# Kernel tuning notes

Measured on AMD Instinct MI355X. Metric: run time of the kernel, lower is better.

Reference implementation:

```python
import jax, jax.numpy as jnp
import numpy as np

NUM_HEADS = 8
DIM_HEAD = 64
HEIGHT_TOP_K = 256
WIDTH_TOP_K = 256


def setup_inputs() -> dict:
    key = jax.random.key(0)
    k1, k2, k3 = jax.random.split(key, 3)
    B, N, C = 4, 2048, 512
    x = jax.random.normal(k1, (B, N, C), dtype=jnp.float32)
    w_qkv = jax.random.normal(k2, (C, 3 * C), dtype=jnp.float32) * (C ** -0.5)
    w_out = jax.random.normal(k3, (C, C), dtype=jnp.float32) * (C ** -0.5)
    b_out = jnp.zeros((C,), dtype=jnp.float32)
    return {"x": x, "w_qkv": w_qkv, "w_out": w_out, "b_out": b_out}


def _topk_mask(scores, k):
    # scores: (B, H, N) -> binary mask (B, H, N) with 1s at top-k positions
    N = scores.shape[-1]
    _, idx = jax.lax.top_k(scores, k)          # (B, H, k)
    # indices are distinct, so summing one-hots == scatter set(1)
    return jax.nn.one_hot(idx, N, dtype=scores.dtype).sum(axis=-2)


def reference(x, w_qkv, w_out, b_out):
    B, N, C = x.shape
    H, D = NUM_HEADS, DIM_HEAD
    scale = D ** -0.5

    qkv = x @ w_qkv                             # (B, N, 3C)
    q, k, v = jnp.split(qkv, 3, axis=-1)
    # (B, N, C) -> (B, H, N, D)
    q = q.reshape(B, N, H, D).transpose(0, 2, 1, 3)
    k = k.reshape(B, N, H, D).transpose(0, 2, 1, 3)
    v = v.reshape(B, N, H, D).transpose(0, 2, 1, 3)

    attn = jnp.einsum('bhid,bhjd->bhij', q, k) * scale   # (B, H, N, N)

    hk = min(HEIGHT_TOP_K, N)
    wk = min(WIDTH_TOP_K, N)
    row_mask = _topk_mask(attn.mean(axis=-1), hk)        # (B, H, N)
    col_mask = _topk_mask(attn.mean(axis=-2), wk)        # (B, H, N)
    attn = attn * row_mask[..., :, None] * col_mask[..., None, :]

    attn = jax.nn.softmax(attn, axis=-1)
    out = jnp.einsum('bhij,bhjd->bhid', attn, v)         # (B, H, N, D)
    out = out.transpose(0, 2, 1, 3).reshape(B, N, C)
    return out @ w_out + b_out
```

## Files before the change

kernel.cpp:

```cpp
#include <hip/hip_runtime.h>
#include <math.h>

#define Bsz 4
#define Nseq 2048
#define Cdim 512
#define Hn 8
#define Dh 64
#define TK 256
#define BH (Bsz*Hn)
#define QKVC 1536

typedef __attribute__((ext_vector_type(8))) short bf16x8;
typedef __attribute__((ext_vector_type(4))) float f32x4;

__device__ __forceinline__ unsigned short f2bf(float x) {
    unsigned u = __float_as_uint(x);
    unsigned r = (u + 0x7fffu + ((u >> 16) & 1u)) >> 16;
    return (unsigned short)r;
}
__device__ __forceinline__ float bf2f(unsigned short h) {
    return __uint_as_float((unsigned)h << 16);
}

__global__ __launch_bounds__(256) void prep(const float* __restrict__ w_qkv,
                                            bf16x8* __restrict__ hi,
                                            bf16x8* __restrict__ lo,
                                            const float* __restrict__ x,
                                            float* __restrict__ xpart) {
    int bid = blockIdx.x;
    int tid = threadIdx.x;
    if (bid < 384) {
        int nt = bid >> 2;
        int kt = (bid & 3) * 4 + (tid >> 6);
        int lane = tid & 63;
        int c = nt * 16 + (lane & 15);
        int kbase = kt * 32 + (lane >> 4) * 8;
        bf16x8 h, l;
        #pragma unroll
        for (int j = 0; j < 8; ++j) {
            float v = w_qkv[(size_t)(kbase + j) * QKVC + c];
            unsigned short hv = f2bf(v);
            h[j] = (short)hv;
            l[j] = (short)f2bf(v - bf2f(hv));
        }
        int idx = (nt * 16 + kt) * 64 + lane;
        hi[idx] = h;
        lo[idx] = l;
    } else {
        int r = bid - 384;
        int b = r >> 7, rc = r & 127;
        const float* xp = x + ((size_t)b * Nseq + rc * 16) * Cdim;
        float s0 = 0.f, s1 = 0.f;
        #pragma unroll 4
        for (int rr = 0; rr < 16; ++rr) {
            s0 += xp[rr * Cdim + tid];
            s1 += xp[rr * Cdim + 256 + tid];
        }
        xpart[((size_t)b * 128 + rc) * Cdim + tid] = s0;
        xpart[((size_t)b * 128 + rc) * Cdim + 256 + tid] = s1;
    }
}

__global__ __launch_bounds__(256) void statsA(const float* __restrict__ xpart,
                                              const float* __restrict__ w_qkv,
                                              float* __restrict__ spart) {
    int b = blockIdx.x, kc = blockIdx.y, nb = blockIdx.z;
    __shared__ float xr[8][32];
    __shared__ float xs[32];
    int t = threadIdx.x;
    int i = t & 31, g = t >> 5;
    float s = 0.f;
    #pragma unroll 4
    for (int j = 0; j < 16; ++j)
        s += xpart[((size_t)b * 128 + g * 16 + j) * Cdim + kc * 32 + i];
    xr[g][i] = s;
    __syncthreads();
    if (t < 32) {
        float v = 0.f;
        #pragma unroll
        for (int gg = 0; gg < 8; ++gg) v += xr[gg][t];
        xs[t] = v;
    }
    __syncthreads();

    float a0 = 0.f;
    const float* wbase = w_qkv + (size_t)(kc * 32) * QKVC + nb * 256 + t;
    #pragma unroll 4
    for (int i2 = 0; i2 < 32; ++i2)
        a0 += xs[i2] * wbase[(size_t)i2 * QKVC];
    spart[(size_t)(b * 16 + kc) * QKVC + nb * 256 + t] = a0;
}

__global__ __launch_bounds__(256) void statsB(const float* __restrict__ spart,
                                              const float* __restrict__ w_qkv,
                                              float* __restrict__ sv,
                                              float* __restrict__ rvec,
                                              float* __restrict__ cvec) {
    int bh = blockIdx.x, cb = blockIdx.y;
    int b = bh >> 3, h = bh & 7;
    __shared__ float qm[64], km[64];
    int t = threadIdx.x;
    if (t < 192) {
        int which = t >> 6, d = t & 63;
        int col = which * 512 + h * 64 + d;
        float s = 0.f;
        #pragma unroll
        for (int kc = 0; kc < 16; ++kc)
            s += spart[(size_t)(b * 16 + kc) * QKVC + col];
        if (which == 0)      qm[d] = s * (1.0f / Nseq);
        else if (which == 1) km[d] = s * (1.0f / Nseq);
        else if (cb == 0)    sv[bh * 64 + d] = s;
    }
    __syncthreads();
    int c = cb * 256 + t;
    const float4* wr = (const float4*)(w_qkv + (size_t)c * QKVC + h * 64);
    const float4* wc = (const float4*)(w_qkv + (size_t)c * QKVC + 512 + h * 64);
    float r = 0.f, cv = 0.f;
    #pragma unroll
    for (int d4 = 0; d4 < 16; ++d4) {
        float4 w1 = wr[d4], w2 = wc[d4];
        float4 k1 = *(const float4*)&km[d4 * 4];
        float4 q1 = *(const float4*)&qm[d4 * 4];
        r  += w1.x * k1.x + w1.y * k1.y + w1.z * k1.z + w1.w * k1.w;
        cv += w2.x * q1.x + w2.y * q1.y + w2.z * q1.z + w2.w * q1.w;
    }
    rvec[(size_t)bh * Cdim + c] = r;
    cvec[(size_t)bh * Cdim + c] = cv;
}

__global__ __launch_bounds__(256) void score3_kernel(const float* __restrict__ x,
                                                     const float* __restrict__ rvec,
                                                     const float* __restrict__ cvec,
                                                     float* __restrict__ rsc,
                                                     float* __restrict__ csc) {
    int b = blockIdx.x, rc = blockIdx.y, half = blockIdx.z;
    __shared__ float vs[8 * 8 * 68];
    int t = threadIdx.x;
    int r = t >> 3, g = t & 7;

    const float4* xp = (const float4*)(x + ((size_t)b * Nseq + rc * 32 + r) * Cdim + g * 64);
    float4 xr[16];
    #pragma unroll
    for (int j4 = 0; j4 < 16; ++j4) xr[j4] = xp[j4];

    {
        const float* src = half ? cvec : rvec;
        const float4* sp = (const float4*)(src + (size_t)b * 8 * Cdim);
        for (int i = t; i < 8 * 128; i += 256) {
            int v = i >> 7, c4 = i & 127;
            float4 val = sp[v * 128 + c4];
            int gg = c4 >> 4, j4 = c4 & 15;
            *(float4*)&vs[(v * 8 + gg) * 68 + j4 * 4] = val;
        }
    }
    __syncthreads();

    float acc[8];
    #pragma unroll
    for (int v = 0; v < 8; ++v) acc[v] = 0.f;
    #pragma unroll
    for (int j4 = 0; j4 < 16; ++j4) {
        float4 xv = xr[j4];
        #pragma unroll
        for (int v = 0; v < 8; ++v) {
            float4 wv = *(const float4*)&vs[(v * 8 + g) * 68 + j4 * 4];
            acc[v] += xv.x * wv.x + xv.y * wv.y + xv.z * wv.z + xv.w * wv.w;
        }
    }
    #pragma unroll
    for (int v = 0; v < 8; ++v) {
        float s = acc[v];
        s += __shfl_xor(s, 1, 64);
        s += __shfl_xor(s, 2, 64);
        s += __shfl_xor(s, 4, 64);
        acc[v] = s;
    }
    if (g == 0) {
        int i = rc * 32 + r;
        float* outp = half ? csc : rsc;
        #pragma unroll
        for (int v = 0; v < 8; ++v)
            outp[(size_t)(b * 8 + v) * Nseq + i] = acc[v] * 0.125f;
    }
}

__global__ __launch_bounds__(256) void topk4(const float* __restrict__ rsc,
                                             const float* __restrict__ csc,
                                             int* __restrict__ ridx,
                                             int* __restrict__ cidx,
                                             int* __restrict__ rankmap) {
    int selid = blockIdx.x;
    int bh = selid >> 1, which = selid & 1;
    const float* sin = which ? (csc + (size_t)bh * Nseq) : (rsc + (size_t)bh * Nseq);
    __shared__ int hist[256];
    __shared__ int sS[256];
    __shared__ int tieidx[2048];
    __shared__ int sh_D, sh_above, sh_tiecnt;
    int tid = threadIdx.x;

    unsigned k[8];
    #pragma unroll
    for (int j = 0; j < 8; ++j) {
        unsigned u = __float_as_uint(sin[j * 256 + tid]);
        k[j] = (u & 0x80000000u) ? ~u : (u | 0x80000000u);
    }

    unsigned pref = 0;
    int above = 0;
    for (int level = 3; level >= 0; --level) {
        hist[tid] = 0;
        __syncthreads();
        int sh = level * 8;
        #pragma unroll
        for (int j = 0; j < 8; ++j) {
            bool match;
            if (level == 3) match = true;
            else            match = ((k[j] >> (sh + 8)) == pref);
            if (match) atomicAdd(&hist[(k[j] >> sh) & 255], 1);
        }
        __syncthreads();
        sS[tid] = hist[tid];
        __syncthreads();
        for (int off = 1; off < 256; off <<= 1) {
            int v = (tid + off < 256) ? sS[tid + off] : 0;
            __syncthreads();
            sS[tid] += v;
            __syncthreads();
        }
        int Sincl = sS[tid];
        int Sexcl = (tid < 255) ? sS[tid + 1] : 0;
        if (above + Sexcl < TK && above + Sincl >= TK) {
            sh_D = tid;
            sh_above = above + Sexcl;
        }
        __syncthreads();
        pref = (pref << 8) | (unsigned)sh_D;
        above = sh_above;
        __syncthreads();
    }
    unsigned T = pref;
    int rem = TK - above;

    if (tid == 0) sh_tiecnt = 0;
    __syncthreads();
    int cnt = 0;
    #pragma unroll
    for (int j = 0; j < 8; ++j) {
        if (k[j] > T) ++cnt;
        if (k[j] == T) {
            int p = atomicAdd(&sh_tiecnt, 1);
            tieidx[p] = j * 256 + tid;
        }
    }
    sS[tid] = cnt;
    __syncthreads();
    for (int off = 1; off < 256; off <<= 1) {
        int v = (tid >= off) ? sS[tid - off] : 0;
        __syncthreads();
        sS[tid] += v;
        __syncthreads();
    }
    int base = sS[tid] - cnt;
    int tc = sh_tiecnt;
    int* outp = which ? (cidx + bh * TK) : (ridx + bh * TK);
    #pragma unroll
    for (int j = 0; j < 8; ++j) {
        int i = j * 256 + tid;
        int r = -1;
        if (k[j] > T) {
            r = base++;
        } else if (k[j] == T) {
            int rk = 0;
            for (int t2 = 0; t2 < tc; ++t2) rk += (tieidx[t2] < i) ? 1 : 0;
            if (rk < rem) r = above + rk;
        }
        if (r >= 0) outp[r] = i;
        if (which == 0) rankmap[(size_t)bh * Nseq + i] = r;
    }
}

__device__ __forceinline__ f32x4 mfma16(bf16x8 a, bf16x8 b, f32x4 c) {
    return __builtin_amdgcn_mfma_f32_16x16x32_bf16(a, b, c, 0, 0, 0);
}

__global__ __launch_bounds__(256) void selgemm3(const float* __restrict__ x,
                                                const int* __restrict__ ridx,
                                                const int* __restrict__ cidx,
                                                const bf16x8* __restrict__ Bph,
                                                const bf16x8* __restrict__ Bpl,
                                                float* __restrict__ qsel,
                                                float* __restrict__ ksel,
                                                float* __restrict__ vsel) {
    int mq = blockIdx.x, part = blockIdx.y, bh = blockIdx.z;
    int b = bh >> 3, h = bh & 7;
    int tid = threadIdx.x;
    int wv = tid >> 6, lane = tid & 63;
    const int* idxp = (part == 0 ? ridx : cidx) + bh * TK + mq * 64 + wv * 16;
    int row = idxp[lane & 15];
    const float* ap = x + ((size_t)b * Nseq + row) * Cdim + (lane >> 4) * 8;
    size_t orow = (size_t)bh * TK + mq * 64 + wv * 16;
    int nt0 = (part == 0) ? (h * 4) : (part == 1 ? (32 + h * 4) : (64 + h * 4));
    float* outp = (part == 0) ? qsel : (part == 1 ? ksel : vsel);

    f32x4 acc[4];
    #pragma unroll
    for (int i = 0; i < 4; ++i) acc[i] = (f32x4){0.f, 0.f, 0.f, 0.f};
    float4 a0 = *(const float4*)ap;
    float4 a1 = *(const float4*)(ap + 4);
    #pragma unroll 2
    for (int kt = 0; kt < 16; ++kt) {
        float4 na0 = a0, na1 = a1;
        if (kt < 15) {
            na0 = *(const float4*)(ap + (kt + 1) * 32);
            na1 = *(const float4*)(ap + (kt + 1) * 32 + 4);
        }
        float vv[8] = {a0.x, a0.y, a0.z, a0.w, a1.x, a1.y, a1.z, a1.w};
        bf16x8 ah, al;
        #pragma unroll
        for (int j = 0; j < 8; ++j) {
            unsigned short hv = f2bf(vv[j]);
            ah[j] = (short)hv;
            al[j] = (short)f2bf(vv[j] - bf2f(hv));
        }
        #pragma unroll
        for (int ni = 0; ni < 4; ++ni) {
            int nt16 = nt0 + ni;
            bf16x8 bh8 = Bph[((size_t)nt16 * 16 + kt) * 64 + lane];
            bf16x8 bl8 = Bpl[((size_t)nt16 * 16 + kt) * 64 + lane];
            acc[ni] = mfma16(ah, bh8, acc[ni]);
            acc[ni] = mfma16(ah, bl8, acc[ni]);
            acc[ni] = mfma16(al, bh8, acc[ni]);
        }
        a0 = na0; a1 = na1;
    }
    int cl = lane & 15, rq = (lane >> 4) * 4;
    #pragma unroll
    for (int ni = 0; ni < 4; ++ni) {
        int csub = ni * 16 + cl;
        #pragma unroll
        for (int r = 0; r < 4; ++r)
            outp[(orow + rq + r) * 64 + csub] = acc[ni][r];
    }
}

__global__ __launch_bounds__(256) void attn_fused3(const float* __restrict__ qsel,
                                                   const float* __restrict__ ksel,
                                                   const float* __restrict__ vsel,
                                                   const float* __restrict__ sv,
                                                   float* __restrict__ delta) {
    int bh = blockIdx.x;
    int rblk = blockIdx.y;
    __shared__ float Kt[64 * 256];
    __shared__ float Qs[16 * 64];
    __shared__ float umS[16], izS[16];
    int tid = threadIdx.x;
    {
        int j = tid;
        const float4* kp4 = (const float4*)(ksel + ((size_t)bh * TK + j) * 64);
        #pragma unroll
        for (int d4 = 0; d4 < 16; ++d4) {
            float4 kv = kp4[d4];
            Kt[(d4 * 4 + 0) * 256 + j] = kv.x;
            Kt[(d4 * 4 + 1) * 256 + j] = kv.y;
            Kt[(d4 * 4 + 2) * 256 + j] = kv.z;
            Kt[(d4 * 4 + 3) * 256 + j] = kv.w;
        }
    }
    for (int idx = tid; idx < 16 * 64; idx += 256)
        Qs[idx] = qsel[((size_t)bh * TK + rblk * 16) * 64 + idx];
    __syncthreads();

    int wave = tid >> 6, lane = tid & 63;
    int iw0 = wave * 4;
    float e[4][4];
    #pragma unroll
    for (int r = 0; r < 4; ++r)
        #pragma unroll
        for (int t = 0; t < 4; ++t) e[r][t] = 0.f;
    #pragma unroll 8
    for (int d = 0; d < 64; ++d) {
        float4 kv = *(const float4*)&Kt[d * 256 + 4 * lane];
        #pragma unroll
        for (int r = 0; r < 4; ++r) {
            float qd = Qs[(iw0 + r) * 64 + d];
            e[r][0] += qd * kv.x; e[r][1] += qd * kv.y;
            e[r][2] += qd * kv.z; e[r][3] += qd * kv.w;
        }
    }
    #pragma unroll
    for (int r = 0; r < 4; ++r) {
        float s0 = e[r][0] * 0.125f, s1 = e[r][1] * 0.125f;
        float s2 = e[r][2] * 0.125f, s3 = e[r][3] * 0.125f;
        float mx = fmaxf(fmaxf(s0, s1), fmaxf(s2, s3));
        #pragma unroll
        for (int off = 32; off; off >>= 1) mx = fmaxf(mx, __shfl_xor(mx, off, 64));
        mx = fmaxf(mx, 0.0f);
        float e0 = __expf(s0 - mx), e1 = __expf(s1 - mx);
        float e2 = __expf(s2 - mx), e3 = __expf(s3 - mx);
        float zs = e0 + e1 + e2 + e3;
        #pragma unroll
        for (int off = 32; off; off >>= 1) zs += __shfl_xor(zs, off, 64);
        if (lane == 0) {
            float em = __expf(-mx);
            umS[iw0 + r] = em;
            izS[iw0 + r] = 1.0f / ((float)(Nseq - TK) * em + zs);
        }
        e[r][0] = e0; e[r][1] = e1; e[r][2] = e2; e[r][3] = e3;
    }
    __syncthreads();
    float* E = Kt;
    #pragma unroll
    for (int r = 0; r < 4; ++r)
        *(float4*)&E[(iw0 + r) * 256 + 4 * lane] = (float4){e[r][0], e[r][1], e[r][2], e[r][3]};
    __syncthreads();

    const float* vbase = vsel + (size_t)bh * TK * 64 + lane;
    float ssel = 0.f;
    float acc[4];
    #pragma unroll
    for (int r = 0; r < 4; ++r) acc[r] = 0.f;
    #pragma unroll 4
    for (int j = 0; j < TK; ++j) {
        float v = vbase[j * 64];
        ssel += v;
        #pragma unroll
        for (int r = 0; r < 4; ++r)
            acc[r] += E[(iw0 + r) * 256 + j] * v;
    }
    float svd = sv[bh * 64 + lane];
    float sadj = svd - ssel;
    float uval = svd * (1.0f / Nseq);
    #pragma unroll
    for (int r = 0; r < 4; ++r) {
        int i = rblk * 16 + iw0 + r;
        float outv = (umS[iw0 + r] * sadj + acc[r]) * izS[iw0 + r];
        delta[((size_t)bh * TK + i) * 64 + lane] = outv - uval;
    }
}

__global__ __launch_bounds__(256) void deltamm_ub(const float* __restrict__ delta,
                                                  const float* __restrict__ w_out,
                                                  const float* __restrict__ b_out,
                                                  const float* __restrict__ sv,
                                                  float* __restrict__ deltaout,
                                                  float* __restrict__ ubase) {
    int bid = blockIdx.x;
    int tid = threadIdx.x;
    if (bid < 512) {
        int bh = bid >> 4, sub = bid & 15;
        int rh = sub >> 2, ct = sub & 3;
        int h = bh & 7;
        __shared__ float As[64][65];
        __shared__ float Ws[64][132];
        for (int idx = tid; idx < 64 * 64; idx += 256) {
            int row = idx >> 6, k = idx & 63;
            As[row][k] = delta[((size_t)bh * TK + rh * 64 + row) * 64 + k];
        }
        for (int idx = tid; idx < 64 * 128; idx += 256) {
            int k = idx >> 7, c = idx & 127;
            Ws[k][c] = w_out[(size_t)(h * 64 + k) * 512 + ct * 128 + c];
        }
        __syncthreads();
        int tx = tid & 15, ty = tid >> 4;
        float acc[4][8];
        #pragma unroll
        for (int r = 0; r < 4; ++r)
            #pragma unroll
            for (int c = 0; c < 8; ++c) acc[r][c] = 0.f;
        for (int k = 0; k < 64; ++k) {
            float a[4], bv[8];
            #pragma unroll
            for (int r = 0; r < 4; ++r) a[r] = As[ty * 4 + r][k];
            #pragma unroll
            for (int cc = 0; cc < 4; ++cc) {
                bv[cc]     = Ws[k][tx * 4 + cc];
                bv[4 + cc] = Ws[k][64 + tx * 4 + cc];
            }
            #pragma unroll
            for (int r = 0; r < 4; ++r)
                #pragma unroll
                for (int c = 0; c < 8; ++c) acc[r][c] += a[r] * bv[c];
        }
        #pragma unroll
        for (int r = 0; r < 4; ++r) {
            size_t ro = ((size_t)bh * TK + rh * 64 + ty * 4 + r) * 512 + ct * 128;
            #pragma unroll
            for (int cc = 0; cc < 4; ++cc) {
                deltaout[ro + tx * 4 + cc]      = acc[r][cc];
                deltaout[ro + 64 + tx * 4 + cc] = acc[r][4 + cc];
            }
        }
    } else {
        int r2 = bid - 512;
        int b = r2 >> 3;
        int c0 = (r2 & 7) * 64;
        int c = tid & 63, kg = tid >> 6;
        float s = 0.f;
        for (int k = kg * 128; k < kg * 128 + 128; ++k) {
            float hu = sv[(b * 8 + (k >> 6)) * 64 + (k & 63)] * (1.0f / Nseq);
            s += hu * w_out[(size_t)k * 512 + c0 + c];
        }
        __shared__ float red[4][64];
        red[kg][c] = s;
        __syncthreads();
        if (tid < 64)
            ubase[b * 512 + c0 + c] = red[0][c] + red[1][c] + red[2][c] + red[3][c] + b_out[c0 + c];
    }
}

__global__ __launch_bounds__(256) void compose(const float* __restrict__ ubase,
                                               const int* __restrict__ rankmap,
                                               const float* __restrict__ deltaout,
                                               float* __restrict__ out) {
    int r0 = blockIdx.x * 4;
    int b = r0 >> 11;
    int tid = threadIdx.x;
    float u0 = ubase[b * 512 + tid];
    float u1 = ubase[b * 512 + 256 + tid];
    for (int rr = 0; rr < 4; ++rr) {
        int i = (r0 + rr) & 2047;
        float a0 = u0, a1 = u1;
        #pragma unroll
        for (int h = 0; h < 8; ++h) {
            int rk = rankmap[(size_t)(b * 8 + h) * Nseq + i];
            if (rk >= 0) {
                const float* dp = deltaout + ((size_t)(b * 8 + h) * TK + rk) * 512;
                a0 += dp[tid];
                a1 += dp[256 + tid];
            }
        }
        float* op = out + ((size_t)b * Nseq + i) * 512;
        op[tid] = a0;
        op[256 + tid] = a1;
    }
}

extern "C" void kernel_launch(void* const* d_in, const int* in_sizes, int n_in,
                              void* d_out, int out_size, void* d_ws, size_t ws_size,
                              hipStream_t stream) {
    const float* x     = (const float*)d_in[0];
    const float* w_qkv = (const float*)d_in[1];
    const float* w_out = (const float*)d_in[2];
    const float* b_out = (const float*)d_in[3];
    float* out = (float*)d_out;

    float* ws = (float*)d_ws;
    float* xpart   = ws;
    float* spart   = xpart + 262144;
    float* sv      = spart + 98304;
    float* rvec    = sv + 2048;
    float* cvec    = rvec + 16384;
    float* rsc     = cvec + 16384;
    float* csc     = rsc + 65536;
    int*   ridx    = (int*)(csc + 65536);
    int*   cidx    = ridx + 8192;
    int*   rankmap = cidx + 8192;
    float* ubase   = (float*)(rankmap + 65536);
    bf16x8* Bp_hi  = (bf16x8*)(ubase + 2048);
    bf16x8* Bp_lo  = (bf16x8*)((float*)Bp_hi + 393216);
    float* qsel    = (float*)Bp_lo + 393216;
    float* ksel    = qsel + 524288;
    float* vsel    = ksel + 524288;
    float* delta   = vsel + 524288;
    float* deltaout = delta + 524288;

    prep<<<896, 256, 0, stream>>>(w_qkv, Bp_hi, Bp_lo, x, xpart);
    statsA<<<dim3(Bsz, 16, 6), 256, 0, stream>>>(xpart, w_qkv, spart);
    statsB<<<dim3(BH, 2), 256, 0, stream>>>(spart, w_qkv, sv, rvec, cvec);
    score3_kernel<<<dim3(Bsz, 64, 2), 256, 0, stream>>>(x, rvec, cvec, rsc, csc);
    topk4<<<BH * 2, 256, 0, stream>>>(rsc, csc, ridx, cidx, rankmap);
    selgemm3<<<dim3(4, 3, BH), 256, 0, stream>>>(x, ridx, cidx, Bp_hi, Bp_lo, qsel, ksel, vsel);
    attn_fused3<<<dim3(BH, 16), 256, 0, stream>>>(qsel, ksel, vsel, sv, delta);
    deltamm_ub<<<544, 256, 0, stream>>>(delta, w_out, b_out, sv, deltaout, ubase);
    compose<<<Bsz * Nseq / 4, 256, 0, stream>>>(ubase, rankmap, deltaout, out);
}
```

Baseline: 172.5 us.

## Fuse all pipeline stages into one cooperative persistent kernel with grid syncs

Turns each of the nine stage kernels into a device function and runs them in sequence inside one cooperative kernel. Stages are separated by grid.sync, and blocks stride over each stage's work units. Shared memory is a union of the per-stage layouts. This removes eight kernel launch gaps and their tail drains, at the cost of grid-wide barriers, occupancy being capped by the largest shared-memory footprint (the attention stage's 68KB), and fewer blocks than some stages have work units. If the cooperative launch fails, the separate kernels are launched as before.

```diff
diff --git a/kernel.cpp b/kernel.cpp
--- a/kernel.cpp
+++ b/kernel.cpp
@@ -1,5 +1,8 @@
 #include <hip/hip_runtime.h>
+#include <hip/hip_cooperative_groups.h>
 #include <math.h>
+
+namespace cg = cooperative_groups;
 
 #define Bsz 4
 #define Nseq 2048
@@ -21,17 +24,28 @@
 __device__ __forceinline__ float bf2f(unsigned short h) {
     return __uint_as_float((unsigned)h << 16);
 }
-
-__global__ __launch_bounds__(256) void prep(const float* __restrict__ w_qkv,
-                                            bf16x8* __restrict__ hi,
-                                            bf16x8* __restrict__ lo,
-                                            const float* __restrict__ x,
-                                            float* __restrict__ xpart) {
-    int bid = blockIdx.x;
+__device__ __forceinline__ f32x4 mfma16(bf16x8 a, bf16x8 b, f32x4 c) {
+    return __builtin_amdgcn_mfma_f32_16x16x32_bf16(a, b, c, 0, 0, 0);
+}
+
+struct S2Sh { float xr[8][32]; float xs[32]; };
+struct S3Sh { float qm[64]; float km[64]; };
+struct S4Sh { float vs[8 * 8 * 68]; };
+struct S5Sh { int hist[256]; int sS[256]; int tieidx[2048]; int D; int above; int tiecnt; };
+struct S7Sh { float Kt[64 * 256]; float Qs[16 * 64]; float umS[16]; float izS[16]; };
+struct S8Sh { float As[64][65]; float Ws[64][132]; float red[4][64]; };
+union FusedSh {
+    S2Sh s2; S3Sh s3; S4Sh s4; S5Sh s5; S7Sh s7; S8Sh s8;
+};
+
+
+__device__ void prep_body(int u, const float* __restrict__ w_qkv,
+                          bf16x8* __restrict__ hi, bf16x8* __restrict__ lo,
+                          const float* __restrict__ x, float* __restrict__ xpart) {
     int tid = threadIdx.x;
-    if (bid < 384) {
-        int nt = bid >> 2;
-        int kt = (bid & 3) * 4 + (tid >> 6);
+    if (u < 384) {
+        int nt = u >> 2;
+        int kt = (u & 3) * 4 + (tid >> 6);
         int lane = tid & 63;
         int c = nt * 16 + (lane & 15);
         int kbase = kt * 32 + (lane >> 4) * 8;
@@ -47,7 +61,7 @@
         hi[idx] = h;
         lo[idx] = l;
     } else {
-        int r = bid - 384;
+        int r = u - 384;
         int b = r >> 7, rc = r & 127;
         const float* xp = x + ((size_t)b * Nseq + rc * 16) * Cdim;
         float s0 = 0.f, s1 = 0.f;
@@ -61,55 +75,50 @@
     }
 }
 
-__global__ __launch_bounds__(256) void statsA(const float* __restrict__ xpart,
-                                              const float* __restrict__ w_qkv,
-                                              float* __restrict__ spart) {
-    int b = blockIdx.x, kc = blockIdx.y, nb = blockIdx.z;
-    __shared__ float xr[8][32];
-    __shared__ float xs[32];
+__device__ void statsA_body(int u, const float* __restrict__ xpart,
+                            const float* __restrict__ w_qkv,
+                            float* __restrict__ spart, S2Sh& s) {
+    int b = u & 3, kc = (u >> 2) & 15, nb = u >> 6;
     int t = threadIdx.x;
     int i = t & 31, g = t >> 5;
-    float s = 0.f;
+    float acc = 0.f;
     #pragma unroll 4
     for (int j = 0; j < 16; ++j)
-        s += xpart[((size_t)b * 128 + g * 16 + j) * Cdim + kc * 32 + i];
-    xr[g][i] = s;
+        acc += xpart[((size_t)b * 128 + g * 16 + j) * Cdim + kc * 32 + i];
+    s.xr[g][i] = acc;
     __syncthreads();
     if (t < 32) {
         float v = 0.f;
         #pragma unroll
-        for (int gg = 0; gg < 8; ++gg) v += xr[gg][t];
-        xs[t] = v;
-    }
-    __syncthreads();
-
+        for (int gg = 0; gg < 8; ++gg) v += s.xr[gg][t];
+        s.xs[t] = v;
+    }
+    __syncthreads();
     float a0 = 0.f;
     const float* wbase = w_qkv + (size_t)(kc * 32) * QKVC + nb * 256 + t;
     #pragma unroll 4
     for (int i2 = 0; i2 < 32; ++i2)
-        a0 += xs[i2] * wbase[(size_t)i2 * QKVC];
+        a0 += s.xs[i2] * wbase[(size_t)i2 * QKVC];
     spart[(size_t)(b * 16 + kc) * QKVC + nb * 256 + t] = a0;
 }
 
-__global__ __launch_bounds__(256) void statsB(const float* __restrict__ spart,
-                                              const float* __restrict__ w_qkv,
-                                              float* __restrict__ sv,
-                                              float* __restrict__ rvec,
-                                              float* __restrict__ cvec) {
-    int bh = blockIdx.x, cb = blockIdx.y;
+__device__ void statsB_body(int u, const float* __restrict__ spart,
+                            const float* __restrict__ w_qkv,
+                            float* __restrict__ sv, float* __restrict__ rvec,
+                            float* __restrict__ cvec, S3Sh& s) {
+    int bh = u & 31, cb = u >> 5;
     int b = bh >> 3, h = bh & 7;
-    __shared__ float qm[64], km[64];
     int t = threadIdx.x;
     if (t < 192) {
         int which = t >> 6, d = t & 63;
         int col = which * 512 + h * 64 + d;
-        float s = 0.f;
+        float sm = 0.f;
         #pragma unroll
         for (int kc = 0; kc < 16; ++kc)
-            s += spart[(size_t)(b * 16 + kc) * QKVC + col];
-        if (which == 0)      qm[d] = s * (1.0f / Nseq);
-        else if (which == 1) km[d] = s * (1.0f / Nseq);
-        else if (cb == 0)    sv[bh * 64 + d] = s;
+            sm += spart[(size_t)(b * 16 + kc) * QKVC + col];
+        if (which == 0)      s.qm[d] = sm * (1.0f / Nseq);
+        else if (which == 1) s.km[d] = sm * (1.0f / Nseq);
+        else if (cb == 0)    sv[bh * 64 + d] = sm;
     }
     __syncthreads();
     int c = cb * 256 + t;
@@ -119,8 +128,8 @@
     #pragma unroll
     for (int d4 = 0; d4 < 16; ++d4) {
         float4 w1 = wr[d4], w2 = wc[d4];
-        float4 k1 = *(const float4*)&km[d4 * 4];
-        float4 q1 = *(const float4*)&qm[d4 * 4];
+        float4 k1 = *(const float4*)&s.km[d4 * 4];
+        float4 q1 = *(const float4*)&s.qm[d4 * 4];
         r  += w1.x * k1.x + w1.y * k1.y + w1.z * k1.z + w1.w * k1.w;
         cv += w2.x * q1.x + w2.y * q1.y + w2.z * q1.z + w2.w * q1.w;
     }
@@ -128,21 +137,18 @@
     cvec[(size_t)bh * Cdim + c] = cv;
 }
 
-__global__ __launch_bounds__(256) void score3_kernel(const float* __restrict__ x,
-                                                     const float* __restrict__ rvec,
-                                                     const float* __restrict__ cvec,
-                                                     float* __restrict__ rsc,
-                                                     float* __restrict__ csc) {
-    int b = blockIdx.x, rc = blockIdx.y, half = blockIdx.z;
-    __shared__ float vs[8 * 8 * 68];
+__device__ void score3_body(int u, const float* __restrict__ x,
+                            const float* __restrict__ rvec,
+                            const float* __restrict__ cvec,
+                            float* __restrict__ rsc, float* __restrict__ csc,
+                            S4Sh& s) {
+    int b = u & 3, rc = (u >> 2) & 63, half = u >> 8;
     int t = threadIdx.x;
     int r = t >> 3, g = t & 7;
-
     const float4* xp = (const float4*)(x + ((size_t)b * Nseq + rc * 32 + r) * Cdim + g * 64);
     float4 xr[16];
     #pragma unroll
     for (int j4 = 0; j4 < 16; ++j4) xr[j4] = xp[j4];
-
     {
         const float* src = half ? cvec : rvec;
         const float4* sp = (const float4*)(src + (size_t)b * 8 * Cdim);
@@ -150,11 +156,10 @@
             int v = i >> 7, c4 = i & 127;
             float4 val = sp[v * 128 + c4];
             int gg = c4 >> 4, j4 = c4 & 15;
-            *(float4*)&vs[(v * 8 + gg) * 68 + j4 * 4] = val;
-        }
-    }
-    __syncthreads();
-
+            *(float4*)&s.vs[(v * 8 + gg) * 68 + j4 * 4] = val;
+        }
+    }
+    __syncthreads();
     float acc[8];
     #pragma unroll
     for (int v = 0; v < 8; ++v) acc[v] = 0.f;
@@ -163,17 +168,17 @@
         float4 xv = xr[j4];
         #pragma unroll
         for (int v = 0; v < 8; ++v) {
-            float4 wv = *(const float4*)&vs[(v * 8 + g) * 68 + j4 * 4];
+            float4 wv = *(const float4*)&s.vs[(v * 8 + g) * 68 + j4 * 4];
             acc[v] += xv.x * wv.x + xv.y * wv.y + xv.z * wv.z + xv.w * wv.w;
         }
     }
     #pragma unroll
     for (int v = 0; v < 8; ++v) {
-        float s = acc[v];
-        s += __shfl_xor(s, 1, 64);
-        s += __shfl_xor(s, 2, 64);
-        s += __shfl_xor(s, 4, 64);
-        acc[v] = s;
+        float sm = acc[v];
+        sm += __shfl_xor(sm, 1, 64);
+        sm += __shfl_xor(sm, 2, 64);
+        sm += __shfl_xor(sm, 4, 64);
+        acc[v] = sm;
     }
     if (g == 0) {
         int i = rc * 32 + r;
@@ -184,31 +189,23 @@
     }
 }
 
-__global__ __launch_bounds__(256) void topk4(const float* __restrict__ rsc,
-                                             const float* __restrict__ csc,
-                                             int* __restrict__ ridx,
-                                             int* __restrict__ cidx,
-                                             int* __restrict__ rankmap) {
-    int selid = blockIdx.x;
-    int bh = selid >> 1, which = selid & 1;
+__device__ void topk4_body(int u, const float* __restrict__ rsc,
+                           const float* __restrict__ csc,
+                           int* __restrict__ ridx, int* __restrict__ cidx,
+                           int* __restrict__ rankmap, S5Sh& s) {
+    int bh = u >> 1, which = u & 1;
     const float* sin = which ? (csc + (size_t)bh * Nseq) : (rsc + (size_t)bh * Nseq);
-    __shared__ int hist[256];
-    __shared__ int sS[256];
-    __shared__ int tieidx[2048];
-    __shared__ int sh_D, sh_above, sh_tiecnt;
     int tid = threadIdx.x;
-
     unsigned k[8];
     #pragma unroll
     for (int j = 0; j < 8; ++j) {
-        unsigned u = __float_as_uint(sin[j * 256 + tid]);
-        k[j] = (u & 0x80000000u) ? ~u : (u | 0x80000000u);
-    }
-
+        unsigned uu = __float_as_uint(sin[j * 256 + tid]);
+        k[j] = (uu & 0x80000000u) ? ~uu : (uu | 0x80000000u);
+    }
     unsigned pref = 0;
     int above = 0;
     for (int level = 3; level >= 0; --level) {
-        hist[tid] = 0;
+        s.hist[tid] = 0;
         __syncthreads();
         int sh = level * 8;
         #pragma unroll
@@ -216,52 +213,51 @@
             bool match;
             if (level == 3) match = true;
             else            match = ((k[j] >> (sh + 8)) == pref);
-            if (match) atomicAdd(&hist[(k[j] >> sh) & 255], 1);
-        }
-        __syncthreads();
-        sS[tid] = hist[tid];
+            if (match) atomicAdd(&s.hist[(k[j] >> sh) & 255], 1);
+        }
+        __syncthreads();
+        s.sS[tid] = s.hist[tid];
         __syncthreads();
         for (int off = 1; off < 256; off <<= 1) {
-            int v = (tid + off < 256) ? sS[tid + off] : 0;
+            int v = (tid + off < 256) ? s.sS[tid + off] : 0;
             __syncthreads();
-            sS[tid] += v;
+            s.sS[tid] += v;
             __syncthreads();
         }
-        int Sincl = sS[tid];
-        int Sexcl = (tid < 255) ? sS[tid + 1] : 0;
+        int Sincl = s.sS[tid];
+        int Sexcl = (tid < 255) ? s.sS[tid + 1] : 0;
         if (above + Sexcl < TK && above + Sincl >= TK) {
-            sh_D = tid;
-            sh_above = above + Sexcl;
-        }
-        __syncthreads();
-        pref = (pref << 8) | (unsigned)sh_D;
-        above = sh_above;
+            s.D = tid;
+            s.above = above + Sexcl;
+        }
+        __syncthreads();
+        pref = (pref << 8) | (unsigned)s.D;
+        above = s.above;
         __syncthreads();
     }
     unsigned T = pref;
     int rem = TK - above;
-
-    if (tid == 0) sh_tiecnt = 0;
+    if (tid == 0) s.tiecnt = 0;
     __syncthreads();
     int cnt = 0;
     #pragma unroll
     for (int j = 0; j < 8; ++j) {
         if (k[j] > T) ++cnt;
         if (k[j] == T) {
-            int p = atomicAdd(&sh_tiecnt, 1);
-            tieidx[p] = j * 256 + tid;
-        }
-    }
-    sS[tid] = cnt;
+            int p = atomicAdd(&s.tiecnt, 1);
+            s.tieidx[p] = j * 256 + tid;
+        }
+    }
+    s.sS[tid] = cnt;
     __syncthreads();
     for (int off = 1; off < 256; off <<= 1) {
-        int v = (tid >= off) ? sS[tid - off] : 0;
-        __syncthreads();
-        sS[tid] += v;
-        __syncthreads();
-    }
-    int base = sS[tid] - cnt;
-    int tc = sh_tiecnt;
+        int v = (tid >= off) ? s.sS[tid - off] : 0;
+        __syncthreads();
+        s.sS[tid] += v;
+        __syncthreads();
+    }
+    int base = s.sS[tid] - cnt;
+    int tc = s.tiecnt;
     int* outp = which ? (cidx + bh * TK) : (ridx + bh * TK);
     #pragma unroll
     for (int j = 0; j < 8; ++j) {
@@ -271,7 +267,7 @@
             r = base++;
         } else if (k[j] == T) {
             int rk = 0;
-            for (int t2 = 0; t2 < tc; ++t2) rk += (tieidx[t2] < i) ? 1 : 0;
+            for (int t2 = 0; t2 < tc; ++t2) rk += (s.tieidx[t2] < i) ? 1 : 0;
             if (rk < rem) r = above + rk;
         }
         if (r >= 0) outp[r] = i;
@@ -279,19 +275,15 @@
     }
 }
 
-__device__ __forceinline__ f32x4 mfma16(bf16x8 a, bf16x8 b, f32x4 c) {
-    return __builtin_amdgcn_mfma_f32_16x16x32_bf16(a, b, c, 0, 0, 0);
-}
-
-__global__ __launch_bounds__(256) void selgemm3(const float* __restrict__ x,
-                                                const int* __restrict__ ridx,
-                                                const int* __restrict__ cidx,
-                                                const bf16x8* __restrict__ Bph,
-                                                const bf16x8* __restrict__ Bpl,
-                                                float* __restrict__ qsel,
-                                                float* __restrict__ ksel,
-                                                float* __restrict__ vsel) {
-    int mq = blockIdx.x, part = blockIdx.y, bh = blockIdx.z;
+__device__ void selgemm3_body(int u, const float* __restrict__ x,
+                              const int* __restrict__ ridx,
+                              const int* __restrict__ cidx,
+                              const bf16x8* __restrict__ Bph,
+                              const bf16x8* __restrict__ Bpl,
+                              float* __restrict__ qsel,
+                              float* __restrict__ ksel,
+                              float* __restrict__ vsel) {
+    int mq = u & 3, part = (u >> 2) % 3, bh = (u >> 2) / 3;
     int b = bh >> 3, h = bh & 7;
     int tid = threadIdx.x;
     int wv = tid >> 6, lane = tid & 63;
@@ -343,16 +335,12 @@
     }
 }
 
-__global__ __launch_bounds__(256) void attn_fused3(const float* __restrict__ qsel,
-                                                   const float* __restrict__ ksel,
-                                                   const float* __restrict__ vsel,
-                                                   const float* __restrict__ sv,
-                                                   float* __restrict__ delta) {
-    int bh = blockIdx.x;
-    int rblk = blockIdx.y;
-    __shared__ float Kt[64 * 256];
-    __shared__ float Qs[16 * 64];
-    __shared__ float umS[16], izS[16];
+__device__ void attn_body(int u, const float* __restrict__ qsel,
+                          const float* __restrict__ ksel,
+                          const float* __restrict__ vsel,
+                          const float* __restrict__ sv,
+                          float* __restrict__ delta, S7Sh& s) {
+    int bh = u & 31, rblk = u >> 5;
     int tid = threadIdx.x;
     {
         int j = tid;
@@ -360,14 +348,14 @@
         #pragma unroll
         for (int d4 = 0; d4 < 16; ++d4) {
             float4 kv = kp4[d4];
-            Kt[(d4 * 4 + 0) * 256 + j] = kv.x;
-            Kt[(d4 * 4 + 1) * 256 + j] = kv.y;
-            Kt[(d4 * 4 + 2) * 256 + j] = kv.z;
-            Kt[(d4 * 4 + 3) * 256 + j] = kv.w;
+            s.Kt[(d4 * 4 + 0) * 256 + j] = kv.x;
+            s.Kt[(d4 * 4 + 1) * 256 + j] = kv.y;
+            s.Kt[(d4 * 4 + 2) * 256 + j] = kv.z;
+            s.Kt[(d4 * 4 + 3) * 256 + j] = kv.w;
         }
     }
     for (int idx = tid; idx < 16 * 64; idx += 256)
-        Qs[idx] = qsel[((size_t)bh * TK + rblk * 16) * 64 + idx];
+        s.Qs[idx] = qsel[((size_t)bh * TK + rblk * 16) * 64 + idx];
     __syncthreads();
 
     int wave = tid >> 6, lane = tid & 63;
@@ -379,10 +367,10 @@
         for (int t = 0; t < 4; ++t) e[r][t] = 0.f;
     #pragma unroll 8
     for (int d = 0; d < 64; ++d) {
-        float4 kv = *(const float4*)&Kt[d * 256 + 4 * lane];
+        float4 kv = *(const float4*)&s.Kt[d * 256 + 4 * lane];
         #pragma unroll
         for (int r = 0; r < 4; ++r) {
-            float qd = Qs[(iw0 + r) * 64 + d];
+            float qd = s.Qs[(iw0 + r) * 64 + d];
             e[r][0] += qd * kv.x; e[r][1] += qd * kv.y;
             e[r][2] += qd * kv.z; e[r][3] += qd * kv.w;
         }
@@ -402,13 +390,13 @@
         for (int off = 32; off; off >>= 1) zs += __shfl_xor(zs, off, 64);
         if (lane == 0) {
             float em = __expf(-mx);
-            umS[iw0 + r] = em;
-            izS[iw0 + r] = 1.0f / ((float)(Nseq - TK) * em + zs);
+            s.umS[iw0 + r] = em;
+            s.izS[iw0 + r] = 1.0f / ((float)(Nseq - TK) * em + zs);
         }
         e[r][0] = e0; e[r][1] = e1; e[r][2] = e2; e[r][3] = e3;
     }
     __syncthreads();
-    float* E = Kt;
+    float* E = s.Kt;
     #pragma unroll
     for (int r = 0; r < 4; ++r)
         *(float4*)&E[(iw0 + r) * 256 + 4 * lane] = (float4){e[r][0], e[r][1], e[r][2], e[r][3]};
@@ -433,32 +421,29 @@
     #pragma unroll
     for (int r = 0; r < 4; ++r) {
         int i = rblk * 16 + iw0 + r;
-        float outv = (umS[iw0 + r] * sadj + acc[r]) * izS[iw0 + r];
+        float outv = (s.umS[iw0 + r] * sadj + acc[r]) * s.izS[iw0 + r];
         delta[((size_t)bh * TK + i) * 64 + lane] = outv - uval;
     }
 }
 
-__global__ __launch_bounds__(256) void deltamm_ub(const float* __restrict__ delta,
-                                                  const float* __restrict__ w_out,
-                                                  const float* __restrict__ b_out,
-                                                  const float* __restrict__ sv,
-                                                  float* __restrict__ deltaout,
-                                                  float* __restrict__ ubase) {
-    int bid = blockIdx.x;
+__device__ void deltamm_body(int u, const float* __restrict__ delta,
+                             const float* __restrict__ w_out,
+                             const float* __restrict__ b_out,
+                             const float* __restrict__ sv,
+                             float* __restrict__ deltaout,
+                             float* __restrict__ ubase, S8Sh& s) {
     int tid = threadIdx.x;
-    if (bid < 512) {
-        int bh = bid >> 4, sub = bid & 15;
+    if (u < 512) {
+        int bh = u >> 4, sub = u & 15;
         int rh = sub >> 2, ct = sub & 3;
         int h = bh & 7;
-        __shared__ float As[64][65];
-        __shared__ float Ws[64][132];
         for (int idx = tid; idx < 64 * 64; idx += 256) {
             int row = idx >> 6, k = idx & 63;
-            As[row][k] = delta[((size_t)bh * TK + rh * 64 + row) * 64 + k];
+            s.As[row][k] = delta[((size_t)bh * TK + rh * 64 + row) * 64 + k];
         }
         for (int idx = tid; idx < 64 * 128; idx += 256) {
             int k = idx >> 7, c = idx & 127;
-            Ws[k][c] = w_out[(size_t)(h * 64 + k) * 512 + ct * 128 + c];
+            s.Ws[k][c] = w_out[(size_t)(h * 64 + k) * 512 + ct * 128 + c];
         }
         __syncthreads();
         int tx = tid & 15, ty = tid >> 4;
@@ -470,11 +455,11 @@
         for (int k = 0; k < 64; ++k) {
             float a[4], bv[8];
             #pragma unroll
-            for (int r = 0; r < 4; ++r) a[r] = As[ty * 4 + r][k];
+            for (int r = 0; r < 4; ++r) a[r] = s.As[ty * 4 + r][k];
             #pragma unroll
             for (int cc = 0; cc < 4; ++cc) {
-                bv[cc]     = Ws[k][tx * 4 + cc];
-                bv[4 + cc] = Ws[k][64 + tx * 4 + cc];
+                bv[cc]     = s.Ws[k][tx * 4 + cc];
+                bv[4 + cc] = s.Ws[k][64 + tx * 4 + cc];
             }
             #pragma unroll
             for (int r = 0; r < 4; ++r)
@@ -491,28 +476,27 @@
             }
         }
     } else {
-        int r2 = bid - 512;
+        int r2 = u - 512;
         int b = r2 >> 3;
         int c0 = (r2 & 7) * 64;
         int c = tid & 63, kg = tid >> 6;
-        float s = 0.f;
+        float sm = 0.f;
         for (int k = kg * 128; k < kg * 128 + 128; ++k) {
             float hu = sv[(b * 8 + (k >> 6)) * 64 + (k & 63)] * (1.0f / Nseq);
-            s += hu * w_out[(size_t)k * 512 + c0 + c];
-        }
-        __shared__ float red[4][64];
-        red[kg][c] = s;
+            sm += hu * w_out[(size_t)k * 512 + c0 + c];
+        }
+        s.red[kg][c] = sm;
         __syncthreads();
         if (tid < 64)
-            ubase[b * 512 + c0 + c] = red[0][c] + red[1][c] + red[2][c] + red[3][c] + b_out[c0 + c];
-    }
-}
-
-__global__ __launch_bounds__(256) void compose(const float* __restrict__ ubase,
-                                               const int* __restrict__ rankmap,
-                                               const float* __restrict__ deltaout,
-                                               float* __restrict__ out) {
-    int r0 = blockIdx.x * 4;
+            ubase[b * 512 + c0 + c] = s.red[0][c] + s.red[1][c] + s.red[2][c] + s.red[3][c] + b_out[c0 + c];
+    }
+}
+
+__device__ void compose_body(int u, const float* __restrict__ ubase,
+                             const int* __restrict__ rankmap,
+                             const float* __restrict__ deltaout,
+                             float* __restrict__ out) {
+    int r0 = u * 4;
     int b = r0 >> 11;
     int tid = threadIdx.x;
     float u0 = ubase[b * 512 + tid];
@@ -533,6 +517,104 @@
         op[tid] = a0;
         op[256 + tid] = a1;
     }
+}
+
+__global__ __launch_bounds__(256) void prep_k(const float* w_qkv, bf16x8* hi, bf16x8* lo,
+                                              const float* x, float* xpart) {
+    prep_body(blockIdx.x, w_qkv, hi, lo, x, xpart);
+}
+__global__ __launch_bounds__(256) void statsA_k(const float* xpart, const float* w_qkv, float* spart) {
+    __shared__ S2Sh s;
+    statsA_body(blockIdx.x, xpart, w_qkv, spart, s);
+}
+__global__ __launch_bounds__(256) void statsB_k(const float* spart, const float* w_qkv,
+                                                float* sv, float* rvec, float* cvec) {
+    __shared__ S3Sh s;
+    statsB_body(blockIdx.x, spart, w_qkv, sv, rvec, cvec, s);
+}
+__global__ __launch_bounds__(256) void score3_k(const float* x, const float* rvec, const float* cvec,
+                                                float* rsc, float* csc) {
+    __shared__ S4Sh s;
+    score3_body(blockIdx.x, x, rvec, cvec, rsc, csc, s);
+}
+__global__ __launch_bounds__(256) void topk4_k(const float* rsc, const float* csc,
+                                               int* ridx, int* cidx, int* rankmap) {
+    __shared__ S5Sh s;
+    topk4_body(blockIdx.x, rsc, csc, ridx, cidx, rankmap, s);
+}
+__global__ __launch_bounds__(256) void selgemm3_k(const float* x, const int* ridx, const int* cidx,
+                                                  const bf16x8* Bph, const bf16x8* Bpl,
+                                                  float* qsel, float* ksel, float* vsel) {
+    selgemm3_body(blockIdx.x, x, ridx, cidx, Bph, Bpl, qsel, ksel, vsel);
+}
+__global__ __launch_bounds__(256) void attn_k(const float* qsel, const float* ksel, const float* vsel,
+                                              const float* sv, float* delta) {
+    __shared__ S7Sh s;
+    attn_body(blockIdx.x, qsel, ksel, vsel, sv, delta, s);
+}
+__global__ __launch_bounds__(256) void deltamm_k(const float* delta, const float* w_out,
+                                                 const float* b_out, const float* sv,
+                                                 float* deltaout, float* ubase) {
+    __shared__ S8Sh s;
+    deltamm_body(blockIdx.x, delta, w_out, b_out, sv, deltaout, ubase, s);
+}
+__global__ __launch_bounds__(256) void compose_k(const float* ubase, const int* rankmap,
+                                                 const float* deltaout, float* out) {
+    compose_body(blockIdx.x, ubase, rankmap, deltaout, out);
+}
+
+struct Params {
+    const float* x; const float* w_qkv; const float* w_out; const float* b_out;
+    float* out;
+    float* xpart; float* spart; float* sv; float* rvec; float* cvec;
+    float* rsc; float* csc; int* ridx; int* cidx; int* rankmap; float* ubase;
+    const bf16x8* Bph; const bf16x8* Bpl;
+    bf16x8* BphW; bf16x8* BplW;
+    float* qsel; float* ksel; float* vsel; float* delta; float* deltaout;
+};
+
+__global__ __launch_bounds__(256, 2) void fused_all(Params p) {
+    cg::grid_group grid = cg::this_grid();
+    __shared__ FusedSh sh;
+    int nb = gridDim.x;
+    for (int u = blockIdx.x; u < 896; u += nb)
+        prep_body(u, p.w_qkv, p.BphW, p.BplW, p.x, p.xpart);
+    grid.sync();
+    for (int u = blockIdx.x; u < 384; u += nb) {
+        statsA_body(u, p.xpart, p.w_qkv, p.spart, sh.s2);
+        __syncthreads();
+    }
+    grid.sync();
+    for (int u = blockIdx.x; u < 64; u += nb) {
+        statsB_body(u, p.spart, p.w_qkv, p.sv, p.rvec, p.cvec, sh.s3);
+        __syncthreads();
+    }
+    grid.sync();
+    for (int u = blockIdx.x; u < 512; u += nb) {
+        score3_body(u, p.x, p.rvec, p.cvec, p.rsc, p.csc, sh.s4);
+        __syncthreads();
+    }
+    grid.sync();
+    for (int u = blockIdx.x; u < 64; u += nb) {
+        topk4_body(u, p.rsc, p.csc, p.ridx, p.cidx, p.rankmap, sh.s5);
+        __syncthreads();
+    }
+    grid.sync();
+    for (int u = blockIdx.x; u < 384; u += nb)
+        selgemm3_body(u, p.x, p.ridx, p.cidx, p.Bph, p.Bpl, p.qsel, p.ksel, p.vsel);
+    grid.sync();
+    for (int u = blockIdx.x; u < 512; u += nb) {
+        attn_body(u, p.qsel, p.ksel, p.vsel, p.sv, p.delta, sh.s7);
+        __syncthreads();
+    }
+    grid.sync();
+    for (int u = blockIdx.x; u < 544; u += nb) {
+        deltamm_body(u, p.delta, p.w_out, p.b_out, p.sv, p.deltaout, p.ubase, sh.s8);
+        __syncthreads();
+    }
+    grid.sync();
+    for (int u = blockIdx.x; u < 2048; u += nb)
+        compose_body(u, p.ubase, p.rankmap, p.deltaout, p.out);
 }
 
 extern "C" void kernel_launch(void* const* d_in, const int* in_sizes, int n_in,
@@ -564,13 +646,34 @@
     float* delta   = vsel + 524288;
     float* deltaout = delta + 524288;
 
-    prep<<<896, 256, 0, stream>>>(w_qkv, Bp_hi, Bp_lo, x, xpart);
-    statsA<<<dim3(Bsz, 16, 6), 256, 0, stream>>>(xpart, w_qkv, spart);
-    statsB<<<dim3(BH, 2), 256, 0, stream>>>(spart, w_qkv, sv, rvec, cvec);
-    score3_kernel<<<dim3(Bsz, 64, 2), 256, 0, stream>>>(x, rvec, cvec, rsc, csc);
-    topk4<<<BH * 2, 256, 0, stream>>>(rsc, csc, ridx, cidx, rankmap);
-    selgemm3<<<dim3(4, 3, BH), 256, 0, stream>>>(x, ridx, cidx, Bp_hi, Bp_lo, qsel, ksel, vsel);
-    attn_fused3<<<dim3(BH, 16), 256, 0, stream>>>(qsel, ksel, vsel, sv, delta);
-    deltamm_ub<<<544, 256, 0, stream>>>(delta, w_out, b_out, sv, deltaout, ubase);
-    compose<<<Bsz * Nseq / 4, 256, 0, stream>>>(ubase, rankmap, deltaout, out);
-}
+    static int fgrid = 0;
+    if (fgrid == 0) {
+        int nb = 0;
+        if (hipOccupancyMaxActiveBlocksPerMultiprocessor(&nb, fused_all, 256, 0) != hipSuccess || nb < 1)
+            nb = 1;
+        fgrid = (nb >= 2) ? 512 : 256;
+    }
+
+    Params P;
+    P.x = x; P.w_qkv = w_qkv; P.w_out = w_out; P.b_out = b_out; P.out = out;
+    P.xpart = xpart; P.spart = spart; P.sv = sv; P.rvec = rvec; P.cvec = cvec;
+    P.rsc = rsc; P.csc = csc; P.ridx = ridx; P.cidx = cidx; P.rankmap = rankmap;
+    P.ubase = ubase; P.Bph = Bp_hi; P.Bpl = Bp_lo; P.BphW = Bp_hi; P.BplW = Bp_lo;
+    P.qsel = qsel; P.ksel = ksel; P.vsel = vsel; P.delta = delta; P.deltaout = deltaout;
+
+    void* kargs[] = { (void*)&P };
+    hipError_t err = hipLaunchCooperativeKernel((const void*)fused_all,
+                                                dim3(fgrid), dim3(256),
+                                                kargs, 0, stream);
+    if (err != hipSuccess) {
+        prep_k<<<896, 256, 0, stream>>>(w_qkv, Bp_hi, Bp_lo, x, xpart);
+        statsA_k<<<384, 256, 0, stream>>>(xpart, w_qkv, spart);
+        statsB_k<<<64, 256, 0, stream>>>(spart, w_qkv, sv, rvec, cvec);
+        score3_k<<<512, 256, 0, stream>>>(x, rvec, cvec, rsc, csc);
+        topk4_k<<<64, 256, 0, stream>>>(rsc, csc, ridx, cidx, rankmap);
+        selgemm3_k<<<384, 256, 0, stream>>>(x, ridx, cidx, Bp_hi, Bp_lo, qsel, ksel, vsel);
+        attn_k<<<512, 256, 0, stream>>>(qsel, ksel, vsel, sv, delta);
+        deltamm_k<<<544, 256, 0, stream>>>(delta, w_out, b_out, sv, deltaout, ubase);
+        compose_k<<<2048, 256, 0, stream>>>(ubase, rankmap, deltaout, out);
+    }
+}
```

Result: slower. 494.2 us (+186.4%).
